# Optimization experiments

Measured on AMD Instinct MI355X. Metric: run time of the kernel, lower is better.

The kernel has to match this reference:

```python
import jax, jax.numpy as jnp
import numpy as np

N_NODES = 100_000
N_INC = 400_000
N_EDGES = 20_000
N_GRAPHS = 512
N_SEQ = 16
SEQ_LEN = 32
F_IN = 128
HIDDEN = 256
HEADS = 4
OUT = HIDDEN // HEADS  # 64 per head, concat -> HIDDEN
RNN_H = 256
OUT_DIM = 128
NEG_SLOPE = 0.2


def setup_inputs() -> dict:
    key = jax.random.key(0)
    ks = jax.random.split(key, 20)
    p = lambda i, shape: jax.random.normal(ks[i], shape, jnp.float32) * 0.05
    return {
        "x": jax.random.normal(ks[0], (N_NODES, F_IN), jnp.float32),
        "he_node": jax.random.randint(ks[1], (N_INC,), 0, N_NODES),
        "he_edge": jax.random.randint(ks[2], (N_INC,), 0, N_EDGES),
        "batch": jnp.sort(jax.random.randint(ks[3], (N_NODES,), 0, N_GRAPHS)),
        "w_lin": p(4, (F_IN, HIDDEN)),
        "att": p(5, (HEADS, 2 * OUT)),
        "bias": p(6, (HIDDEN,)),
        "w_ih0": p(7, (2, 4 * RNN_H, HIDDEN)),
        "w_hh0": p(8, (2, 4 * RNN_H, RNN_H)),
        "b_ih0": p(9, (2, 4 * RNN_H)),
        "b_hh0": p(10, (2, 4 * RNN_H)),
        "w_ih1": p(11, (2, 4 * RNN_H, 2 * RNN_H)),
        "w_hh1": p(12, (2, 4 * RNN_H, RNN_H)),
        "b_ih1": p(13, (2, 4 * RNN_H)),
        "b_hh1": p(14, (2, 4 * RNN_H)),
        "w_causal": p(15, (2 * RNN_H, HIDDEN)),
        "b_causal": p(16, (HIDDEN,)),
        "w_link": p(17, (HIDDEN, OUT_DIM)),
        "b_link": p(18, (OUT_DIM,)),
    }


def _segment_softmax(logits, seg, num_segments):
    m = jax.ops.segment_max(logits, seg, num_segments)
    m = jnp.where(jnp.isfinite(m), m, 0.0)
    e = jnp.exp(logits - m[seg])
    s = jax.ops.segment_sum(e, seg, num_segments)
    return e / jnp.maximum(s[seg], 1e-16)


def hypergraph_conv(x, he_node, he_edge, w_lin, att, bias):
    # PyG HypergraphConv, use_attention=True, attention_mode='node'.
    xh = (x @ w_lin).reshape(-1, HEADS, OUT)  # [N,H,O]
    ones_inc = jnp.ones((N_INC,), x.dtype)
    cnt_e = jax.ops.segment_sum(ones_inc, he_edge, N_EDGES)  # hyperedge sizes
    # hyperedge_attr = mean of incident raw node features, then shared lin
    eattr = jax.ops.segment_sum(x[he_node], he_edge, N_EDGES) / jnp.maximum(cnt_e, 1.0)[:, None]
    eh = (eattr @ w_lin).reshape(-1, HEADS, OUT)  # [M,H,O]
    x_i = xh[he_node]  # [E,H,O]
    e_j = eh[he_edge]  # [E,H,O]
    alpha = jnp.einsum("ehd,hd->eh", jnp.concatenate([x_i, e_j], axis=-1), att)
    alpha = jax.nn.leaky_relu(alpha, NEG_SLOPE)
    alpha = _segment_softmax(alpha, he_edge, N_EDGES)  # softmax within each hyperedge
    Binv = jnp.where(cnt_e > 0, 1.0 / cnt_e, 0.0)  # hyperedge degree norm
    deg = jax.ops.segment_sum(ones_inc, he_node, N_NODES)
    Dinv = jnp.where(deg > 0, 1.0 / deg, 0.0)  # node degree norm
    # node -> hyperedge, then hyperedge -> node, attention applied both hops
    out_e = Binv[:, None, None] * jax.ops.segment_sum(alpha[:, :, None] * x_i, he_edge, N_EDGES)
    out_n = Dinv[:, None, None] * jax.ops.segment_sum(alpha[:, :, None] * out_e[he_edge], he_node, N_NODES)
    return out_n.reshape(-1, HIDDEN) + bias


def _lstm_dir(xs, w_ih, w_hh, b_ih, b_hh, reverse):
    # xs: [T,B,I]; torch gate order i,f,g,o
    B = xs.shape[1]
    H = w_hh.shape[1]
    def step(carry, x_t):
        h, c = carry
        g = x_t @ w_ih.T + h @ w_hh.T + b_ih + b_hh
        i, f, gg, o = jnp.split(g, 4, axis=-1)
        c = jax.nn.sigmoid(f) * c + jax.nn.sigmoid(i) * jnp.tanh(gg)
        h = jax.nn.sigmoid(o) * jnp.tanh(c)
        return (h, c), h
    h0 = jnp.zeros((B, H), xs.dtype)
    _, hs = jax.lax.scan(step, (h0, h0), xs, reverse=reverse)
    return hs


def bilstm(x_seq, w_ih, w_hh, b_ih, b_hh):
    xs = jnp.swapaxes(x_seq, 0, 1)  # [T,B,I]
    fwd = _lstm_dir(xs, w_ih[0], w_hh[0], b_ih[0], b_hh[0], False)
    bwd = _lstm_dir(xs, w_ih[1], w_hh[1], b_ih[1], b_hh[1], True)
    return jnp.swapaxes(jnp.concatenate([fwd, bwd], axis=-1), 0, 1)


def reference(x, he_node, he_edge, batch, w_lin, att, bias,
              w_ih0, w_hh0, b_ih0, b_hh0, w_ih1, w_hh1, b_ih1, b_hh1,
              w_causal, b_causal, w_link, b_link):
    h = jax.nn.relu(hypergraph_conv(x, he_node, he_edge, w_lin, att, bias))  # [N,HIDDEN]
    cnt_g = jax.ops.segment_sum(jnp.ones((N_NODES,), h.dtype), batch, N_GRAPHS)
    pooled = jax.ops.segment_sum(h, batch, N_GRAPHS) / jnp.maximum(cnt_g, 1.0)[:, None]
    seq = pooled.reshape(N_SEQ, SEQ_LEN, HIDDEN)  # equal-length sequences of graphs
    l1 = bilstm(seq, w_ih0, w_hh0, b_ih0, b_hh0)   # [S,T,2*RNN_H]
    l2 = bilstm(l1, w_ih1, w_hh1, b_ih1, b_hh1)
    causal = jax.nn.relu(l2 @ w_causal + b_causal)
    return jax.nn.sigmoid(causal @ w_link + b_link)  # [S,T,OUT_DIM]
```

## Files before the change

### kernel.cpp

```cpp
#include <hip/hip_runtime.h>
#include <math.h>

#define N_NODES  100000
#define N_INC    400000
#define N_EDGES  20000
#define N_GRAPHS 512
#define F_IN     128
#define HID      256
#define RNN_H    256
#define ODIM     128

__global__ void k_count(const int* __restrict__ he_node, const int* __restrict__ he_edge,
                        int* __restrict__ cnt_e, int* __restrict__ deg) {
  int i = blockIdx.x * 256 + threadIdx.x;
  if (i >= N_INC) return;
  atomicAdd(&cnt_e[he_edge[i]], 1);
  atomicAdd(&deg[he_node[i]], 1);
}

__global__ __launch_bounds__(1024)
void k_scan(const int* __restrict__ cnt, int* __restrict__ start, int n) {
  __shared__ int part[1024];
  int tid = threadIdx.x;
  int chunk = (n + 1023) / 1024;
  int lo = tid * chunk; if (lo > n) lo = n;
  int hi = lo + chunk;  if (hi > n) hi = n;
  int s = 0;
  for (int i = lo; i < hi; ++i) s += cnt[i];
  part[tid] = s;
  __syncthreads();
  for (int off = 1; off < 1024; off <<= 1) {
    int v = (tid >= off) ? part[tid - off] : 0;
    __syncthreads();
    part[tid] += v;
    __syncthreads();
  }
  int run = (tid == 0) ? 0 : part[tid - 1];
  for (int i = lo; i < hi; ++i) { start[i] = run; run += cnt[i]; }
  if (tid == 1023) start[n] = part[1023];
}

__global__ void k_fill(const int* __restrict__ he_node, const int* __restrict__ he_edge,
                       const int* __restrict__ e_start, const int* __restrict__ n_start,
                       int* __restrict__ cur_e, int* __restrict__ cur_n,
                       int* __restrict__ e_idx, int* __restrict__ n_idx) {
  int i = blockIdx.x * 256 + threadIdx.x;
  if (i >= N_INC) return;
  int e = he_edge[i]; int p = atomicAdd(&cur_e[e], 1); e_idx[e_start[e] + p] = i;
  int nn = he_node[i]; int q = atomicAdd(&cur_n[nn], 1); n_idx[n_start[nn] + q] = i;
}

__global__ void k_transpose(const float* __restrict__ in, float* __restrict__ out,
                            int rows, int cols) {
  int idx = blockIdx.x * 256 + threadIdx.x;
  if (idx >= rows * cols) return;
  int r = idx / cols, c = idx - r * cols;
  out[c * rows + r] = in[idx];
}

template<int TT, int TR>
__global__ __launch_bounds__(256)
void k_gemm(const float* __restrict__ A, const float* __restrict__ WT,
            float* __restrict__ C, int M, int N, int K,
            const float* __restrict__ bias1, const float* __restrict__ bias2,
            int act, int remap) {
  __shared__ float As[TT][64];
  __shared__ float Ws[TT][64];
  const int m0 = blockIdx.y * TT, n0 = blockIdx.x * TT;
  const int tid = threadIdx.x;
  const int tc = tid & 15, tr = tid >> 4;
  float acc[TR][TR];
#pragma unroll
  for (int r = 0; r < TR; ++r)
#pragma unroll
    for (int c = 0; c < TR; ++c) acc[r][c] = 0.f;

  for (int kc = 0; kc < K; kc += 64) {
    for (int it = tid; it < TT * 16; it += 256) {
      int r = it >> 4, c4 = it & 15;
      int sw = ((c4 ^ (r >> 3)) & 15) << 2;
      int row = m0 + r;
      float4 v = {0.f, 0.f, 0.f, 0.f};
      if (row < M) v = *(const float4*)&A[(size_t)row * K + kc + c4 * 4];
      *(float4*)&As[r][sw] = v;
      float4 wv = *(const float4*)&WT[(size_t)(n0 + r) * K + kc + c4 * 4];
      *(float4*)&Ws[r][sw] = wv;
    }
    __syncthreads();
#pragma unroll 4
    for (int k4 = 0; k4 < 16; ++k4) {
      float4 wv[TR], av[TR];
#pragma unroll
      for (int c = 0; c < TR; ++c) {
        int rw = tc * TR + c;
        wv[c] = *(const float4*)&Ws[rw][((k4 ^ (rw >> 3)) & 15) << 2];
      }
#pragma unroll
      for (int r = 0; r < TR; ++r) {
        int ra = tr * TR + r;
        av[r] = *(const float4*)&As[ra][((k4 ^ (ra >> 3)) & 15) << 2];
      }
#pragma unroll
      for (int r = 0; r < TR; ++r)
#pragma unroll
        for (int c = 0; c < TR; ++c)
          acc[r][c] += av[r].x * wv[c].x + av[r].y * wv[c].y +
                       av[r].z * wv[c].z + av[r].w * wv[c].w;
    }
    __syncthreads();
  }

#pragma unroll
  for (int r = 0; r < TR; ++r) {
    int row = m0 + tr * TR + r;
    if (row >= M) continue;
    int orow = remap ? ((row & 15) * 32 + (row >> 4)) : row;
#pragma unroll
    for (int c4 = 0; c4 < TR; c4 += 4) {
      float4 o;
      float* op = &o.x;
#pragma unroll
      for (int c = 0; c < 4; ++c) {
        int col = n0 + tc * TR + c4 + c;
        float v = acc[r][c4 + c] +
                  (bias1 ? bias1[col] : 0.f) + (bias2 ? bias2[col] : 0.f);
        if (act == 1) v = fmaxf(v, 0.f);
        else if (act == 2) v = 1.f / (1.f + expf(-v));
        op[c] = v;
      }
      *(float4*)&C[(size_t)orow * N + n0 + tc * TR + c4] = o;
    }
  }
}

__global__ __launch_bounds__(256)
void k_eattr(const float* __restrict__ x, const int* __restrict__ he_node,
             const int* __restrict__ e_start, const int* __restrict__ e_idx,
             float* __restrict__ eattr) {
  int m = blockIdx.x * 4 + (threadIdx.x >> 6);
  if (m >= N_EDGES) return;
  int lane = threadIdx.x & 63;
  int c4 = lane & 31, jp = lane >> 5;
  int begin = e_start[m], end = e_start[m + 1];
  float4 acc = {0.f, 0.f, 0.f, 0.f};
  for (int j = begin + jp; j < end; j += 2) {
    float4 v = *(const float4*)&x[(size_t)he_node[e_idx[j]] * F_IN + c4 * 4];
    acc.x += v.x; acc.y += v.y; acc.z += v.z; acc.w += v.w;
  }
  acc.x += __shfl_xor(acc.x, 32); acc.y += __shfl_xor(acc.y, 32);
  acc.z += __shfl_xor(acc.z, 32); acc.w += __shfl_xor(acc.w, 32);
  if (jp == 0) {
    float inv = 1.f / fmaxf((float)(end - begin), 1.f);
    float4 o = {acc.x * inv, acc.y * inv, acc.z * inv, acc.w * inv};
    *(float4*)&eattr[(size_t)m * F_IN + c4 * 4] = o;
  }
}

__global__ __launch_bounds__(256)
void k_dot(const float* __restrict__ X, const float* __restrict__ att,
           float* __restrict__ s, int half, int nrows) {
  int row = blockIdx.x * 4 + (threadIdx.x >> 6);
  if (row >= nrows) return;
  int lane = threadIdx.x & 63;
  int h = lane >> 4;
  float4 v = *(const float4*)&X[(size_t)row * HID + lane * 4];
  float4 a = *(const float4*)&att[h * 128 + half * 64 + (lane & 15) * 4];
  float p = v.x * a.x + v.y * a.y + v.z * a.z + v.w * a.w;
  p += __shfl_xor(p, 1); p += __shfl_xor(p, 2);
  p += __shfl_xor(p, 4); p += __shfl_xor(p, 8);
  if ((lane & 15) == 0) s[(size_t)row * 4 + h] = p;
}

__global__ void k_logit(const int* __restrict__ he_node, const int* __restrict__ he_edge,
                        const float* __restrict__ s_n, const float* __restrict__ s_e,
                        float* __restrict__ alpha) {
  int i = blockIdx.x * 256 + threadIdx.x;
  if (i >= N_INC) return;
  float4 a = *(const float4*)&s_n[(size_t)he_node[i] * 4];
  float4 b = *(const float4*)&s_e[(size_t)he_edge[i] * 4];
  float4 o;
  o.x = a.x + b.x; o.y = a.y + b.y; o.z = a.z + b.z; o.w = a.w + b.w;
  o.x = o.x > 0.f ? o.x : 0.2f * o.x;
  o.y = o.y > 0.f ? o.y : 0.2f * o.y;
  o.z = o.z > 0.f ? o.z : 0.2f * o.z;
  o.w = o.w > 0.f ? o.w : 0.2f * o.w;
  *(float4*)&alpha[(size_t)i * 4] = o;
}

__global__ __launch_bounds__(256)
void k_softmax(const int* __restrict__ e_start, const int* __restrict__ e_idx,
               float* __restrict__ alpha) {
  int m = blockIdx.x * 4 + (threadIdx.x >> 6);
  if (m >= N_EDGES) return;
  int lane = threadIdx.x & 63;
  int begin = e_start[m], end = e_start[m + 1];
  int cnt = end - begin;
  if (cnt == 0) return;
  int nch = (cnt + 63) >> 6;
  float mx[4] = {-1e30f, -1e30f, -1e30f, -1e30f};
  for (int ch = 0; ch < nch; ++ch) {
    int j = begin + ch * 64 + lane;
    if (j < end) {
      float4 a = *(const float4*)&alpha[(size_t)e_idx[j] * 4];
      mx[0] = fmaxf(mx[0], a.x); mx[1] = fmaxf(mx[1], a.y);
      mx[2] = fmaxf(mx[2], a.z); mx[3] = fmaxf(mx[3], a.w);
    }
  }
#pragma unroll
  for (int h = 0; h < 4; ++h)
    for (int off = 32; off; off >>= 1) mx[h] = fmaxf(mx[h], __shfl_xor(mx[h], off));
  float s[4] = {0.f, 0.f, 0.f, 0.f};
  for (int ch = 0; ch < nch; ++ch) {
    int j = begin + ch * 64 + lane;
    if (j < end) {
      int i = e_idx[j];
      float4 a = *(const float4*)&alpha[(size_t)i * 4];
      a.x = expf(a.x - mx[0]); a.y = expf(a.y - mx[1]);
      a.z = expf(a.z - mx[2]); a.w = expf(a.w - mx[3]);
      *(float4*)&alpha[(size_t)i * 4] = a;
      s[0] += a.x; s[1] += a.y; s[2] += a.z; s[3] += a.w;
    }
  }
#pragma unroll
  for (int h = 0; h < 4; ++h) {
    for (int off = 32; off; off >>= 1) s[h] += __shfl_xor(s[h], off);
    s[h] = 1.f / fmaxf(s[h], 1e-16f);
  }
  for (int ch = 0; ch < nch; ++ch) {
    int j = begin + ch * 64 + lane;
    if (j < end) {
      int i = e_idx[j];
      float4 a = *(const float4*)&alpha[(size_t)i * 4];
      a.x *= s[0]; a.y *= s[1]; a.z *= s[2]; a.w *= s[3];
      *(float4*)&alpha[(size_t)i * 4] = a;
    }
  }
}

__global__ __launch_bounds__(256)
void k_out_e(const float* __restrict__ xh, const float* __restrict__ alpha,
             const int* __restrict__ e_start, const int* __restrict__ e_idx,
             const int* __restrict__ he_node, float* __restrict__ out_e) {
  int m = blockIdx.x * 4 + (threadIdx.x >> 6);
  if (m >= N_EDGES) return;
  int lane = threadIdx.x & 63, h = lane >> 4;
  int begin = e_start[m], end = e_start[m + 1];
  float4 acc = {0.f, 0.f, 0.f, 0.f};
  for (int j = begin; j < end; ++j) {
    int i = e_idx[j];
    float a = alpha[(size_t)i * 4 + h];
    float4 v = *(const float4*)&xh[(size_t)he_node[i] * HID + lane * 4];
    acc.x += a * v.x; acc.y += a * v.y; acc.z += a * v.z; acc.w += a * v.w;
  }
  float bi = (end > begin) ? 1.f / (float)(end - begin) : 0.f;
  float4 o = {acc.x * bi, acc.y * bi, acc.z * bi, acc.w * bi};
  *(float4*)&out_e[(size_t)m * HID + lane * 4] = o;
}

__global__ __launch_bounds__(256)
void k_out_n(const float* __restrict__ out_e, const float* __restrict__ alpha,
             const int* __restrict__ n_start, const int* __restrict__ n_idx,
             const int* __restrict__ he_edge, const float* __restrict__ bias,
             float* __restrict__ hout) {
  int n = blockIdx.x * 4 + (threadIdx.x >> 6);
  if (n >= N_NODES) return;
  int lane = threadIdx.x & 63, h = lane >> 4;
  int begin = n_start[n], end = n_start[n + 1];
  float4 acc = {0.f, 0.f, 0.f, 0.f};
  for (int j = begin; j < end; ++j) {
    int i = n_idx[j];
    float a = alpha[(size_t)i * 4 + h];
    float4 v = *(const float4*)&out_e[(size_t)he_edge[i] * HID + lane * 4];
    acc.x += a * v.x; acc.y += a * v.y; acc.z += a * v.z; acc.w += a * v.w;
  }
  float di = (end > begin) ? 1.f / (float)(end - begin) : 0.f;
  float4 bb = *(const float4*)&bias[lane * 4];
  float4 o;
  o.x = fmaxf(acc.x * di + bb.x, 0.f);
  o.y = fmaxf(acc.y * di + bb.y, 0.f);
  o.z = fmaxf(acc.z * di + bb.z, 0.f);
  o.w = fmaxf(acc.w * di + bb.w, 0.f);
  *(float4*)&hout[(size_t)n * HID + lane * 4] = o;
}

__global__ void k_gstart(const int* __restrict__ batch, int* __restrict__ gs) {
  int g = blockIdx.x * 256 + threadIdx.x;
  if (g > N_GRAPHS) return;
  int lo = 0, hi = N_NODES;
  while (lo < hi) { int mid = (lo + hi) >> 1; if (batch[mid] < g) lo = mid + 1; else hi = mid; }
  gs[g] = lo;
}

__global__ __launch_bounds__(256)
void k_pool(const float* __restrict__ h, const int* __restrict__ gs,
            float* __restrict__ pooled) {
  __shared__ float4 part[4][64];
  int g = blockIdx.x, tid = threadIdx.x;
  int rs = tid >> 6, c4 = tid & 63;
  int begin = gs[g], end = gs[g + 1];
  float4 acc = {0.f, 0.f, 0.f, 0.f};
  for (int n = begin + rs; n < end; n += 4) {
    float4 v = *(const float4*)&h[(size_t)n * HID + c4 * 4];
    acc.x += v.x; acc.y += v.y; acc.z += v.z; acc.w += v.w;
  }
  part[rs][c4] = acc;
  __syncthreads();
  if (rs == 0) {
    float4 a = part[0][c4], b = part[1][c4], c = part[2][c4], d = part[3][c4];
    float inv = 1.f / fmaxf((float)(end - begin), 1.f);
    float4 o = {(a.x + b.x + c.x + d.x) * inv, (a.y + b.y + c.y + d.y) * inv,
                (a.z + b.z + c.z + d.z) * inv, (a.w + b.w + c.w + d.w) * inv};
    *(float4*)&pooled[(size_t)g * HID + c4 * 4] = o;
  }
}

__global__ __launch_bounds__(256)
void k_lstm2(const float* __restrict__ xg, const float* __restrict__ w_hh,
             float* __restrict__ out, float* __restrict__ hbuf,
             int* __restrict__ lc, int rst, int rsb) {
  __shared__ float4 ws4[64][64];
  __shared__ float4 hs[16 * 64];
  const int dir = blockIdx.x >> 4, q = blockIdx.x & 15;
  const int tid = threadIdx.x;
  const int l = tid & 63, w = tid >> 6;
  const int ks = l & 3, rg = l >> 2;

  for (int it = tid; it < 4096; it += 256) {
    int row = it >> 6, c4 = it & 63;
    int g = row >> 4, r = row & 15;
    float4 v = *(const float4*)&w_hh[((size_t)dir * 1024 + g * 256 + q * 16 + r) * 256 + c4 * 4];
    ws4[row][c4 ^ ((c4 >> 4) & 3) ^ (r & 7)] = v;
  }
  __syncthreads();

  float cst[4] = {0.f, 0.f, 0.f, 0.f};
  for (int t = 0; t < 32; ++t) {
    const int te = dir ? (31 - t) : t;
    const float* hprev = hbuf + ((size_t)(t & 1) * 2 + dir) * 16 * 256;
    float4 hv0, hv1, hv2, hv3;
    {
      const float* a0 = hprev + (0 * 256 + tid) * 4;
      const float* a1 = hprev + (1 * 256 + tid) * 4;
      const float* a2 = hprev + (2 * 256 + tid) * 4;
      const float* a3 = hprev + (3 * 256 + tid) * 4;
      asm volatile(
        "global_load_dwordx4 %0, %4, off sc0 sc1\n"
        "global_load_dwordx4 %1, %5, off sc0 sc1\n"
        "global_load_dwordx4 %2, %6, off sc0 sc1\n"
        "global_load_dwordx4 %3, %7, off sc0 sc1\n"
        "s_waitcnt vmcnt(0)"
        : "=&v"(hv0), "=&v"(hv1), "=&v"(hv2), "=&v"(hv3)
        : "v"(a0), "v"(a1), "v"(a2), "v"(a3)
        : "memory");
    }
#pragma unroll
    for (int i = 0; i < 4; ++i) {
      int idx = i * 256 + tid;
      int b = idx >> 6, cc = idx & 63;
      float4 hv = (i == 0) ? hv0 : (i == 1) ? hv1 : (i == 2) ? hv2 : hv3;
      hs[b * 64 + (cc ^ ((cc >> 4) & 3))] = hv;
    }
    __syncthreads();

    float acc[4][4];
#pragma unroll
    for (int g = 0; g < 4; ++g)
#pragma unroll
      for (int lb = 0; lb < 4; ++lb) acc[g][lb] = 0.f;
#pragma unroll
    for (int j = 0; j < 16; ++j) {
      int col = ks * 16 + j;
      int u = col ^ ((col >> 4) & 3);
      float4 h4[4];
#pragma unroll
      for (int lb = 0; lb < 4; ++lb)
        h4[lb] = hs[(w * 4 + lb) * 64 + u];
      int csw = col ^ ks ^ (rg & 7);
#pragma unroll
      for (int g = 0; g < 4; ++g) {
        float4 wv = ws4[g * 16 + rg][csw];
#pragma unroll
        for (int lb = 0; lb < 4; ++lb)
          acc[g][lb] += wv.x * h4[lb].x + wv.y * h4[lb].y + wv.z * h4[lb].z + wv.w * h4[lb].w;
      }
    }
#pragma unroll
    for (int g = 0; g < 4; ++g)
#pragma unroll
      for (int lb = 0; lb < 4; ++lb) {
        float v = acc[g][lb];
        v += __shfl_xor(v, 1);
        v += __shfl_xor(v, 2);
        acc[g][lb] = v;
      }
    float hv[4];
#pragma unroll
    for (int lb = 0; lb < 4; ++lb) {
      int b = w * 4 + lb;
      const float* xp = &xg[(size_t)(b * rsb + te * rst) * 2048 + dir * 1024 + q * 16 + rg];
      float gi = acc[0][lb] + xp[0];
      float gf = acc[1][lb] + xp[256];
      float gg = acc[2][lb] + xp[512];
      float go = acc[3][lb] + xp[768];
      gi = 1.f / (1.f + expf(-gi));
      gf = 1.f / (1.f + expf(-gf));
      gg = tanhf(gg);
      go = 1.f / (1.f + expf(-go));
      cst[lb] = gf * cst[lb] + gi * gg;
      hv[lb] = go * tanhf(cst[lb]);
    }
    float* hnext = hbuf + ((size_t)((t + 1) & 1) * 2 + dir) * 16 * 256;
    if (ks == 0) {
#pragma unroll
      for (int lb = 0; lb < 4; ++lb) {
        int b = w * 4 + lb;
        __hip_atomic_store(&hnext[b * 256 + q * 16 + rg], hv[lb],
                           __ATOMIC_RELAXED, __HIP_MEMORY_SCOPE_AGENT);
        out[((size_t)te * 16 + b) * 512 + dir * 256 + q * 16 + rg] = hv[lb];
      }
    }
    if (t < 31) {
      __syncthreads();
      if (tid == 0) {
        __hip_atomic_fetch_add(&lc[dir * 32 + t], 1, __ATOMIC_RELAXED, __HIP_MEMORY_SCOPE_AGENT);
        while (__hip_atomic_load(&lc[dir * 32 + t], __ATOMIC_RELAXED, __HIP_MEMORY_SCOPE_AGENT) < 16)
          __builtin_amdgcn_s_sleep(1);
      }
      __syncthreads();
    } else {
      __syncthreads();
    }
  }
}

extern "C" void kernel_launch(void* const* d_in, const int* in_sizes, int n_in,
                              void* d_out, int out_size, void* d_ws, size_t ws_size,
                              hipStream_t stream) {
  const float* x        = (const float*)d_in[0];
  const int*   he_node  = (const int*)d_in[1];
  const int*   he_edge  = (const int*)d_in[2];
  const int*   batch    = (const int*)d_in[3];
  const float* w_lin    = (const float*)d_in[4];
  const float* att      = (const float*)d_in[5];
  const float* bias     = (const float*)d_in[6];
  const float* w_ih0    = (const float*)d_in[7];
  const float* w_hh0    = (const float*)d_in[8];
  const float* b_ih0    = (const float*)d_in[9];
  const float* b_hh0    = (const float*)d_in[10];
  const float* w_ih1    = (const float*)d_in[11];
  const float* w_hh1    = (const float*)d_in[12];
  const float* b_ih1    = (const float*)d_in[13];
  const float* b_hh1    = (const float*)d_in[14];
  const float* w_causal = (const float*)d_in[15];
  const float* b_causal = (const float*)d_in[16];
  const float* w_link   = (const float*)d_in[17];
  const float* b_link   = (const float*)d_in[18];
  float* out = (float*)d_out;

  char* ws = (char*)d_ws;
  size_t off = 0;
  auto alloc = [&](size_t bytes) -> void* {
    void* p = ws + off;
    off = (off + bytes + 255) & ~(size_t)255;
    return p;
  };
  float* xh      = (float*)alloc((size_t)N_NODES * HID * 4);
  float* eattr   = (float*)alloc((size_t)N_EDGES * F_IN * 4);
  float* eh      = (float*)alloc((size_t)N_EDGES * HID * 4);
  float* alpha   = (float*)alloc((size_t)N_INC * 4 * 4);
  float* out_e   = (float*)alloc((size_t)N_EDGES * HID * 4);
  float* s_n     = (float*)alloc((size_t)N_NODES * 4 * 4);
  float* s_e     = (float*)alloc((size_t)N_EDGES * 4 * 4);
  int*   cnt_e   = (int*)alloc(N_EDGES * 4);
  int*   deg     = (int*)alloc(N_NODES * 4);
  int*   e_start = (int*)alloc((N_EDGES + 1) * 4);
  int*   n_start = (int*)alloc((N_NODES + 1) * 4);
  int*   cur_e   = (int*)alloc(N_EDGES * 4);
  int*   cur_n   = (int*)alloc(N_NODES * 4);
  int*   e_idx   = (int*)alloc(N_INC * 4);
  int*   n_idx   = (int*)alloc(N_INC * 4);
  int*   gstart  = (int*)alloc((N_GRAPHS + 1) * 4);
  float* pooled  = (float*)alloc((size_t)N_GRAPHS * HID * 4);
  float* wlinT   = (float*)alloc((size_t)HID * F_IN * 4);
  float* wcT     = (float*)alloc((size_t)HID * 512 * 4);
  float* wlkT    = (float*)alloc((size_t)ODIM * HID * 4);
  float* xg1     = (float*)alloc((size_t)512 * 2048 * 4);
  float* xg2     = (float*)alloc((size_t)512 * 2048 * 4);
  float* l1      = (float*)alloc((size_t)512 * 512 * 4);
  float* l2      = (float*)alloc((size_t)512 * 512 * 4);
  float* causal  = (float*)alloc((size_t)512 * HID * 4);
  float* hbuf    = (float*)alloc((size_t)2 * 2 * 2 * 16 * 256 * 4);
  int*   lcnt    = (int*)alloc(2 * 64 * 4);

  (void)hipMemsetAsync(cnt_e, 0, N_EDGES * 4, stream);
  (void)hipMemsetAsync(deg,   0, N_NODES * 4, stream);
  (void)hipMemsetAsync(cur_e, 0, N_EDGES * 4, stream);
  (void)hipMemsetAsync(cur_n, 0, N_NODES * 4, stream);
  (void)hipMemsetAsync(hbuf,  0, (size_t)2 * 2 * 2 * 16 * 256 * 4, stream);
  (void)hipMemsetAsync(lcnt,  0, 2 * 64 * 4, stream);

  k_count<<<(N_INC + 255) / 256, 256, 0, stream>>>(he_node, he_edge, cnt_e, deg);
  k_scan<<<1, 1024, 0, stream>>>(cnt_e, e_start, N_EDGES);
  k_scan<<<1, 1024, 0, stream>>>(deg, n_start, N_NODES);
  k_fill<<<(N_INC + 255) / 256, 256, 0, stream>>>(he_node, he_edge, e_start, n_start,
                                                  cur_e, cur_n, e_idx, n_idx);
  k_gstart<<<(N_GRAPHS + 1 + 255) / 256, 256, 0, stream>>>(batch, gstart);
  k_transpose<<<(F_IN * HID + 255) / 256, 256, 0, stream>>>(w_lin, wlinT, F_IN, HID);
  k_transpose<<<(512 * HID + 255) / 256, 256, 0, stream>>>(w_causal, wcT, 512, HID);
  k_transpose<<<(HID * ODIM + 255) / 256, 256, 0, stream>>>(w_link, wlkT, HID, ODIM);

  k_gemm<128, 8><<<dim3(HID / 128, (N_NODES + 127) / 128), 256, 0, stream>>>(
      x, wlinT, xh, N_NODES, HID, F_IN, nullptr, nullptr, 0, 0);
  k_eattr<<<N_EDGES / 4, 256, 0, stream>>>(x, he_node, e_start, e_idx, eattr);
  k_gemm<128, 8><<<dim3(HID / 128, (N_EDGES + 127) / 128), 256, 0, stream>>>(
      eattr, wlinT, eh, N_EDGES, HID, F_IN, nullptr, nullptr, 0, 0);
  k_dot<<<N_NODES / 4, 256, 0, stream>>>(xh, att, s_n, 0, N_NODES);
  k_dot<<<N_EDGES / 4, 256, 0, stream>>>(eh, att, s_e, 1, N_EDGES);
  k_logit<<<(N_INC + 255) / 256, 256, 0, stream>>>(he_node, he_edge, s_n, s_e, alpha);
  k_softmax<<<N_EDGES / 4, 256, 0, stream>>>(e_start, e_idx, alpha);
  k_out_e<<<N_EDGES / 4, 256, 0, stream>>>(xh, alpha, e_start, e_idx, he_node, out_e);
  k_out_n<<<N_NODES / 4, 256, 0, stream>>>(out_e, alpha, n_start, n_idx, he_edge, bias, xh);
  k_pool<<<N_GRAPHS, 256, 0, stream>>>(xh, gstart, pooled);

  k_gemm<64, 4><<<dim3(2048 / 64, 512 / 64), 256, 0, stream>>>(
      pooled, w_ih0, xg1, 512, 2048, HID, b_ih0, b_hh0, 0, 0);
  k_lstm2<<<32, 256, 0, stream>>>(xg1, w_hh0, l1, hbuf, lcnt, 1, 32);
  k_gemm<64, 4><<<dim3(2048 / 64, 512 / 64), 256, 0, stream>>>(
      l1, w_ih1, xg2, 512, 2048, 512, b_ih1, b_hh1, 0, 0);
  k_lstm2<<<32, 256, 0, stream>>>(xg2, w_hh1, l2, hbuf + 2 * 2 * 16 * 256, lcnt + 64, 16, 1);
  k_gemm<64, 4><<<dim3(HID / 64, 512 / 64), 256, 0, stream>>>(
      l2, wcT, causal, 512, HID, 512, b_causal, nullptr, 1, 0);
  k_gemm<64, 4><<<dim3(ODIM / 64, 512 / 64), 256, 0, stream>>>(
      causal, wlkT, out, 512, ODIM, HID, b_link, nullptr, 2, 1);
  (void)in_sizes; (void)n_in; (void)out_size; (void)ws_size;
}
```

Measured before the change: 1.523 ms.

## Replace LSTM grid barrier with per-block timestamp flags and prefetch gate inputs

The cross-block step barrier in the recurrent LSTM kernel is changed. Previously each step did a counter fetch-add, a single-thread spin and a second block barrier. Now each block publishes a per-block step stamp, and a full wavefront polls all 16 stamps before reading the previous hidden state, which removes one __syncthreads and the atomic RMW per step. The input-gate projections xg are loaded before the wait so their latency overlaps the synchronisation. The risk is memory ordering: relaxed stores and loads with no explicit fence guard visibility of the hidden-state writes. Each wave also polls independently, so there is more spin traffic.

```diff
diff --git a/kernel.cpp b/kernel.cpp
--- a/kernel.cpp
+++ b/kernel.cpp
@@ -317,7 +317,7 @@
 __global__ __launch_bounds__(256)
 void k_lstm2(const float* __restrict__ xg, const float* __restrict__ w_hh,
              float* __restrict__ out, float* __restrict__ hbuf,
-             int* __restrict__ lc, int rst, int rsb) {
+             int* __restrict__ stamp, int rst, int rsb) {
   __shared__ float4 ws4[64][64];
   __shared__ float4 hs[16 * 64];
   const int dir = blockIdx.x >> 4, q = blockIdx.x & 15;
@@ -336,6 +336,24 @@
   float cst[4] = {0.f, 0.f, 0.f, 0.f};
   for (int t = 0; t < 32; ++t) {
     const int te = dir ? (31 - t) : t;
+    float xr[4][4];
+#pragma unroll
+    for (int lb = 0; lb < 4; ++lb) {
+      const float* xp = &xg[(size_t)((w * 4 + lb) * rsb + te * rst) * 2048 + dir * 1024 + q * 16 + rg];
+      xr[0][lb] = xp[0];
+      xr[1][lb] = xp[256];
+      xr[2][lb] = xp[512];
+      xr[3][lb] = xp[768];
+    }
+    if (t > 0) {
+      for (;;) {
+        int sv = t;
+        if (l < 16)
+          sv = __hip_atomic_load(&stamp[dir * 16 + l], __ATOMIC_RELAXED, __HIP_MEMORY_SCOPE_AGENT);
+        if (__all(sv >= t)) break;
+        __builtin_amdgcn_s_sleep(1);
+      }
+    }
     const float* hprev = hbuf + ((size_t)(t & 1) * 2 + dir) * 16 * 256;
     float4 hv0, hv1, hv2, hv3;
     {
@@ -396,12 +414,10 @@
     float hv[4];
 #pragma unroll
     for (int lb = 0; lb < 4; ++lb) {
-      int b = w * 4 + lb;
-      const float* xp = &xg[(size_t)(b * rsb + te * rst) * 2048 + dir * 1024 + q * 16 + rg];
-      float gi = acc[0][lb] + xp[0];
-      float gf = acc[1][lb] + xp[256];
-      float gg = acc[2][lb] + xp[512];
-      float go = acc[3][lb] + xp[768];
+      float gi = acc[0][lb] + xr[0][lb];
+      float gf = acc[1][lb] + xr[1][lb];
+      float gg = acc[2][lb] + xr[2][lb];
+      float go = acc[3][lb] + xr[3][lb];
       gi = 1.f / (1.f + expf(-gi));
       gf = 1.f / (1.f + expf(-gf));
       gg = tanhf(gg);
@@ -421,14 +437,9 @@
     }
     if (t < 31) {
       __syncthreads();
-      if (tid == 0) {
-        __hip_atomic_fetch_add(&lc[dir * 32 + t], 1, __ATOMIC_RELAXED, __HIP_MEMORY_SCOPE_AGENT);
-        while (__hip_atomic_load(&lc[dir * 32 + t], __ATOMIC_RELAXED, __HIP_MEMORY_SCOPE_AGENT) < 16)
-          __builtin_amdgcn_s_sleep(1);
-      }
-      __syncthreads();
-    } else {
-      __syncthreads();
+      if (tid == 0)
+        __hip_atomic_store(&stamp[dir * 16 + q], t + 1,
+                           __ATOMIC_RELAXED, __HIP_MEMORY_SCOPE_AGENT);
     }
   }
 }
@@ -490,14 +501,14 @@
   float* l2      = (float*)alloc((size_t)512 * 512 * 4);
   float* causal  = (float*)alloc((size_t)512 * HID * 4);
   float* hbuf    = (float*)alloc((size_t)2 * 2 * 2 * 16 * 256 * 4);
-  int*   lcnt    = (int*)alloc(2 * 64 * 4);
+  int*   lcnt    = (int*)alloc(2 * 32 * 4);
 
   (void)hipMemsetAsync(cnt_e, 0, N_EDGES * 4, stream);
   (void)hipMemsetAsync(deg,   0, N_NODES * 4, stream);
   (void)hipMemsetAsync(cur_e, 0, N_EDGES * 4, stream);
   (void)hipMemsetAsync(cur_n, 0, N_NODES * 4, stream);
   (void)hipMemsetAsync(hbuf,  0, (size_t)2 * 2 * 2 * 16 * 256 * 4, stream);
-  (void)hipMemsetAsync(lcnt,  0, 2 * 64 * 4, stream);
+  (void)hipMemsetAsync(lcnt,  0, 2 * 32 * 4, stream);
 
   k_count<<<(N_INC + 255) / 256, 256, 0, stream>>>(he_node, he_edge, cnt_e, deg);
   k_scan<<<1, 1024, 0, stream>>>(cnt_e, e_start, N_EDGES);
@@ -527,7 +538,7 @@
   k_lstm2<<<32, 256, 0, stream>>>(xg1, w_hh0, l1, hbuf, lcnt, 1, 32);
   k_gemm<64, 4><<<dim3(2048 / 64, 512 / 64), 256, 0, stream>>>(
       l1, w_ih1, xg2, 512, 2048, 512, b_ih1, b_hh1, 0, 0);
-  k_lstm2<<<32, 256, 0, stream>>>(xg2, w_hh1, l2, hbuf + 2 * 2 * 16 * 256, lcnt + 64, 16, 1);
+  k_lstm2<<<32, 256, 0, stream>>>(xg2, w_hh1, l2, hbuf + 2 * 2 * 16 * 256, lcnt + 32, 16, 1);
   k_gemm<64, 4><<<dim3(HID / 64, 512 / 64), 256, 0, stream>>>(
       l2, wcT, causal, 512, HID, 512, b_causal, nullptr, 1, 0);
   k_gemm<64, 4><<<dim3(ODIM / 64, 512 / 64), 256, 0, stream>>>(
```

After: 1.452 ms. 1.05x faster.
